# Kernel tuning notes

Hardware: AMD Instinct MI355X
Metric: run time of the kernel (lower is better)

The kernel has to match this reference:

```python
import jax, jax.numpy as jnp
import numpy as np

N = 50000
E = 800000
D_IN = 128
D_HID = 256


def setup_inputs() -> dict:
    key = jax.random.key(0)
    ks = jax.random.split(key, 9)
    x = jax.random.normal(ks[0], (N, D_IN), dtype=jnp.float32)
    edge_index = jax.random.randint(ks[1], (2, E), 0, N, dtype=jnp.int64)
    edge_weight = jax.random.uniform(ks[2], (E,), dtype=jnp.float32)
    # GCNConv params (lin: y = x @ W.T, plus bias added after aggregation)
    W1 = jax.random.normal(ks[3], (D_HID, D_IN), dtype=jnp.float32) / np.sqrt(D_IN)
    b1 = jnp.zeros((D_HID,), dtype=jnp.float32)
    W2 = jax.random.normal(ks[4], (D_IN, D_HID), dtype=jnp.float32) / np.sqrt(D_HID)
    b2 = jnp.zeros((D_IN,), dtype=jnp.float32)
    gamma = jnp.ones((D_IN,), dtype=jnp.float32)
    beta = jnp.zeros((D_IN,), dtype=jnp.float32)
    return {"x": x, "edge_index": edge_index, "edge_weight": edge_weight,
            "W1": W1, "b1": b1, "W2": W2, "b2": b2,
            "gamma": gamma, "beta": beta}


def _gcn_norm(edge_index, edge_weight, n_nodes):
    # add self loops with weight 1.0 (PyG gcn_norm default)
    loop = jnp.arange(n_nodes, dtype=edge_index.dtype)
    src = jnp.concatenate([edge_index[0], loop])
    dst = jnp.concatenate([edge_index[1], loop])
    w = jnp.concatenate([edge_weight, jnp.ones((n_nodes,), edge_weight.dtype)])
    # symmetric normalization: deg over target index
    deg = jax.ops.segment_sum(w, dst, num_segments=n_nodes)
    dinv = jnp.where(deg > 0, jax.lax.rsqrt(deg), 0.0)
    norm = dinv[src] * w * dinv[dst]
    return src, dst, norm


def _gcn_conv(x, src, dst, norm, W, b, n_nodes):
    h = x @ W.T                                    # [N, out]
    msg = h[src] * norm[:, None]                   # gather + scale [E+N, out]
    out = jax.ops.segment_sum(msg, dst, num_segments=n_nodes)
    return out + b


def reference(x, edge_index, edge_weight, W1, b1, W2, b2, gamma, beta):
    n_nodes = x.shape[0]
    src, dst, norm = _gcn_norm(edge_index, edge_weight, n_nodes)
    h = _gcn_conv(x, src, dst, norm, W1, b1, n_nodes)
    h = jax.nn.relu(h)
    h = _gcn_conv(h, src, dst, norm, W2, b2, n_nodes)
    # LayerNorm over last dim
    mu = jnp.mean(h, axis=-1, keepdims=True)
    var = jnp.mean(jnp.square(h - mu), axis=-1, keepdims=True)
    h = (h - mu) * jax.lax.rsqrt(var + 1e-5) * gamma + beta
    return h
```

## Files before the change

kernel.cpp:

```cpp
#include <hip/hip_runtime.h>

typedef unsigned short ushort_t;
typedef __attribute__((ext_vector_type(8))) short short8;
typedef __attribute__((ext_vector_type(4))) float float4v;

#define MAXDEG 48

__device__ inline float b2f(ushort_t u) {
    unsigned x = ((unsigned)u) << 16;
    return __builtin_bit_cast(float, x);
}
__device__ inline ushort_t f2b(float f) {
    unsigned x = __builtin_bit_cast(unsigned, f);
    unsigned r = (x + 0x7fffu + ((x >> 16) & 1u)) >> 16;
    return (ushort_t)r;
}

__device__ inline void load_edge(const int* __restrict__ ei, int e, int E,
                                 int& s, int& d) {
    int ec = min(e, E - 1);
    int2 c64 = ((const int2*)ei)[ec];
    unsigned long long m = __ballot(c64.y != 0);
    if (m != 0ull) {
        s = ei[ec];
        d = ei[(size_t)E + ec];
    } else {
        s = c64.x;
        d = ((const int2*)ei)[(size_t)E + ec].x;
    }
}


__global__ __launch_bounds__(256) void k_mega(const int* __restrict__ ei,
                                              const float* __restrict__ w,
                                              const float* __restrict__ x,
                                              const float* __restrict__ W1,
                                              const float* __restrict__ W2,
                                              unsigned* packed,
                                              unsigned* __restrict__ edata,
                                              ushort_t* __restrict__ xb,
                                              ushort_t* __restrict__ W1b,
                                              ushort_t* __restrict__ W2b,
                                              int E, int Nn, int gE, int gX) {
    int b = blockIdx.x;
    bool isEdge;
    int widx;
    if (3 * gE <= (int)gridDim.x) {
        if (b < 3 * gE) {
            if (b % 3 == 0) { isEdge = true;  widx = b / 3; }
            else            { isEdge = false; widx = b - b / 3 - 1; }
        } else {
            isEdge = false; widx = b - gE;
        }
    } else {
        isEdge = b < gE;
        widx = isEdge ? b : b - gE;
    }

    if (isEdge) {
        int e = widx * 256 + threadIdx.x;
        int s, d;
        load_edge(ei, e, E, s, d);
        if (e < E) {
            if ((unsigned)s < (unsigned)Nn && (unsigned)d < (unsigned)Nn) {
                float wv = w[e];
                unsigned fx = (unsigned)(wv * 65536.0f + 0.5f);
                unsigned old = atomicAdd(packed + d, (1u << 22) | fx);
                int r = (int)(old >> 22);
                if (r < MAXDEG) {
                    unsigned wq = (unsigned)(wv * 32768.0f + 0.5f);
                    wq = min(wq, 32767u);
                    edata[(size_t)d * MAXDEG + r] = ((unsigned)s << 15) | wq;
                }
            }
        }
    } else if (widx < gX) {
        int i = widx * 256 + threadIdx.x;
        if (i < Nn * 32) {
            float4v v = ((const float4v*)x)[i];
            ushort4 o;
            o.x = f2b(v[0]); o.y = f2b(v[1]); o.z = f2b(v[2]); o.w = f2b(v[3]);
            ((ushort4*)xb)[i] = o;
        }
    } else {
        int i = (widx - gX) * 256 + threadIdx.x;
        if (i < 32768) W1b[i] = f2b(W1[i]);
        else if (i < 65536) W2b[i - 32768] = f2b(W2[i - 32768]);
    }
}


__global__ __launch_bounds__(256) void k_dinv(const unsigned* __restrict__ packed,
                                              float* __restrict__ dinv, int Nn) {
    int i = blockIdx.x * 256 + threadIdx.x;
    if (i < Nn) {
        float wsum = (float)(packed[i] & 0x3FFFFFu) * (1.0f / 65536.0f);
        dinv[i] = rsqrtf(1.0f + wsum);
    }
}


__device__ inline void agg_edges(const ushort_t* __restrict__ src,
                                 const unsigned* __restrict__ ed, int n,
                                 const float* __restrict__ dinv,
                                 int hl, float* a) {
    for (int i = 0; i < n; i += 8) {
        unsigned e2[8];
#pragma unroll
        for (int j = 0; j < 8; ++j) e2[j] = ed[min(i + j, n - 1)];
        ushort4 q[8];
        float nw[8];
#pragma unroll
        for (int j = 0; j < 8; ++j) {
            int sN = (int)(e2[j] >> 15);
            q[j] = ((const ushort4*)(src + (size_t)sN * 128))[hl];
            float d = dinv[sN];
            nw[j] = (i + j < n)
                        ? d * (float)(e2[j] & 0x7FFFu) * (1.0f / 32768.0f)
                        : 0.f;
        }
#pragma unroll
        for (int j = 0; j < 8; ++j) {
            a[0] += b2f(q[j].x) * nw[j]; a[1] += b2f(q[j].y) * nw[j];
            a[2] += b2f(q[j].z) * nw[j]; a[3] += b2f(q[j].w) * nw[j];
        }
    }
}


__global__ __launch_bounds__(256) void k_agg1(const ushort_t* __restrict__ xb,
                                              const unsigned* __restrict__ packed,
                                              const unsigned* __restrict__ edata,
                                              const float* __restrict__ dinv,
                                              ushort_t* __restrict__ ax, int Nn) {
    int v = (blockIdx.x * blockDim.x + threadIdx.x) >> 5;
    int hl = threadIdx.x & 31;
    if (v >= Nn) return;
    float dv = dinv[v];
    ushort4 pq = ((const ushort4*)(xb + (size_t)v * 128))[hl];
    float a[4] = {b2f(pq.x) * dv, b2f(pq.y) * dv, b2f(pq.z) * dv, b2f(pq.w) * dv};
    int n = min((int)(packed[v] >> 22), MAXDEG);
    agg_edges(xb, edata + (size_t)v * MAXDEG, n, dinv, hl, a);
    ushort4 o;
    o.x = f2b(a[0] * dv); o.y = f2b(a[1] * dv);
    o.z = f2b(a[2] * dv); o.w = f2b(a[3] * dv);
    ((ushort4*)(ax + (size_t)v * 128))[hl] = o;
}


__global__ __launch_bounds__(256, 2) void k_gemm_fused(const ushort_t* __restrict__ ax,
                                                       const ushort_t* __restrict__ W1b,
                                                       const float* __restrict__ b1v,
                                                       const ushort_t* __restrict__ W2b,
                                                       ushort_t* __restrict__ h2, int Nn) {
    __shared__ ushort_t tile[64][264];
    int tid = threadIdx.x, wid = tid >> 6, lane = tid & 63;
    int m = lane & 15, q = lane >> 4;
    int blk = blockIdx.x * 64;

    short8 wf[4][4];
#pragma unroll
    for (int nt = 0; nt < 4; ++nt) {
        const ushort_t* wb = W1b + (size_t)(wid * 64 + nt * 16 + m) * 128 + q * 8;
#pragma unroll
        for (int kt = 0; kt < 4; ++kt) wf[nt][kt] = *(const short8*)(wb + kt * 32);
    }
    short8 af[4][4];
#pragma unroll
    for (int mi = 0; mi < 4; ++mi) {
        int arow = blk + mi * 16 + m;
        bool rv = arow < Nn;
        const ushort_t* ab = ax + (size_t)arow * 128 + q * 8;
#pragma unroll
        for (int kt = 0; kt < 4; ++kt)
            af[mi][kt] = rv ? *(const short8*)(ab + kt * 32) : (short8)0;
    }

    float4v acc1[4][4];
#pragma unroll
    for (int mi = 0; mi < 4; ++mi)
#pragma unroll
        for (int nt = 0; nt < 4; ++nt) acc1[mi][nt] = (float4v){0.f, 0.f, 0.f, 0.f};

#pragma unroll
    for (int kt = 0; kt < 4; ++kt)
#pragma unroll
        for (int mi = 0; mi < 4; ++mi)
#pragma unroll
            for (int nt = 0; nt < 4; ++nt)
                acc1[mi][nt] = __builtin_amdgcn_mfma_f32_16x16x32_bf16(
                    af[mi][kt], wf[nt][kt], acc1[mi][nt], 0, 0, 0);

#pragma unroll
    for (int nt = 0; nt < 4; ++nt) {
        int col = wid * 64 + nt * 16 + m;
        float bb = b1v[col];
#pragma unroll
        for (int mi = 0; mi < 4; ++mi) {
#pragma unroll
            for (int r = 0; r < 4; ++r) {
                float v = acc1[mi][nt][r] + bb;
                v = v > 0.f ? v : 0.f;
                tile[mi * 16 + q * 4 + r][col] = f2b(v);
            }
        }
    }
    __syncthreads();

    short8 w2f[2][8];
#pragma unroll
    for (int n2 = 0; n2 < 2; ++n2) {
        const ushort_t* wb = W2b + (size_t)(wid * 32 + n2 * 16 + m) * 256 + q * 8;
#pragma unroll
        for (int kt = 0; kt < 8; ++kt) w2f[n2][kt] = *(const short8*)(wb + kt * 32);
    }

    float4v acc2[4][2];
#pragma unroll
    for (int mi = 0; mi < 4; ++mi)
#pragma unroll
        for (int n2 = 0; n2 < 2; ++n2) acc2[mi][n2] = (float4v){0.f, 0.f, 0.f, 0.f};

#pragma unroll
    for (int kt = 0; kt < 8; ++kt) {
#pragma unroll
        for (int mi = 0; mi < 4; ++mi) {
            short8 a2 = *(const short8*)&tile[mi * 16 + m][kt * 32 + q * 8];
#pragma unroll
            for (int n2 = 0; n2 < 2; ++n2)
                acc2[mi][n2] = __builtin_amdgcn_mfma_f32_16x16x32_bf16(
                    a2, w2f[n2][kt], acc2[mi][n2], 0, 0, 0);
        }
    }

#pragma unroll
    for (int mi = 0; mi < 4; ++mi) {
#pragma unroll
        for (int n2 = 0; n2 < 2; ++n2) {
            int col = wid * 32 + n2 * 16 + m;
#pragma unroll
            for (int r = 0; r < 4; ++r) {
                int row = blk + mi * 16 + q * 4 + r;
                if (row < Nn) h2[(size_t)row * 128 + col] = f2b(acc2[mi][n2][r]);
            }
        }
    }
}


__global__ __launch_bounds__(256) void k_agg2_ln(const ushort_t* __restrict__ h2,
                                                 const unsigned* __restrict__ packed,
                                                 const unsigned* __restrict__ edata,
                                                 const float* __restrict__ dinv,
                                                 const float* __restrict__ b2v,
                                                 const float* __restrict__ gv,
                                                 const float* __restrict__ bev,
                                                 float* __restrict__ out, int Nn) {
    int v = (blockIdx.x * blockDim.x + threadIdx.x) >> 5;
    int hl = threadIdx.x & 31;
    if (v >= Nn) return;
    float dv = dinv[v];
    ushort4 pq = ((const ushort4*)(h2 + (size_t)v * 128))[hl];
    float a[4] = {b2f(pq.x) * dv, b2f(pq.y) * dv, b2f(pq.z) * dv, b2f(pq.w) * dv};
    int n = min((int)(packed[v] >> 22), MAXDEG);
    agg_edges(h2, edata + (size_t)v * MAXDEG, n, dinv, hl, a);

    int d0 = hl * 4;
#pragma unroll
    for (int j = 0; j < 4; ++j) {
        a[j] *= dv;
        a[j] += b2v[d0 + j];
    }

    float ssum = a[0] + a[1] + a[2] + a[3];
    float ssq = a[0] * a[0] + a[1] * a[1] + a[2] * a[2] + a[3] * a[3];
#pragma unroll
    for (int off = 1; off < 32; off <<= 1) {
        ssum += __shfl_xor(ssum, off);
        ssq += __shfl_xor(ssq, off);
    }
    float mu = ssum * (1.0f / 128.0f);
    float var = ssq * (1.0f / 128.0f) - mu * mu;
    float r = rsqrtf(var + 1e-5f);
    float4v o;
#pragma unroll
    for (int j = 0; j < 4; ++j)
        o[j] = (a[j] - mu) * r * gv[d0 + j] + bev[d0 + j];
    ((float4v*)(out + (size_t)v * 128))[hl] = o;
}


extern "C" void kernel_launch(void* const* d_in, const int* in_sizes, int n_in,
                              void* d_out, int out_size, void* d_ws, size_t ws_size,
                              hipStream_t stream) {
    const float* x   = (const float*)d_in[0];
    const int*   ei  = (const int*)d_in[1];
    const float* ew  = (const float*)d_in[2];
    const float* W1  = (const float*)d_in[3];
    const float* b1v = (const float*)d_in[4];
    const float* W2  = (const float*)d_in[5];
    const float* b2v = (const float*)d_in[6];
    const float* gv  = (const float*)d_in[7];
    const float* bev = (const float*)d_in[8];
    float* out = (float*)d_out;

    const int Nn = in_sizes[0] / 128;
    const int E  = in_sizes[2];

    char* base = (char*)d_ws;
    size_t off = 0;
    auto alloc = [&](size_t bytes) {
        char* p = base + off;
        off = (off + bytes + 255) & ~(size_t)255;
        return p;
    };
    unsigned* packed = (unsigned*)alloc((size_t)Nn * 4);
    float*    dinv   = (float*)alloc((size_t)Nn * 4);
    unsigned* edata  = (unsigned*)alloc((size_t)Nn * MAXDEG * 4);
    ushort_t* xb     = (ushort_t*)alloc((size_t)Nn * 128 * 2);
    ushort_t* h2     = (ushort_t*)alloc((size_t)Nn * 128 * 2);
    ushort_t* W1b    = (ushort_t*)alloc(32768 * 2);
    ushort_t* W2b    = (ushort_t*)alloc(32768 * 2);
    ushort_t* ax     = (ushort_t*)d_out;
    (void)ws_size; (void)n_in; (void)out_size;

    int gE = (E + 255) / 256;
    int gX = (Nn * 32 + 255) / 256;
    int gW = (Nn + 7) / 8;
    int gG = (Nn + 63) / 64;
    int gD = (Nn + 255) / 256;

    hipMemsetAsync(packed, 0, (size_t)Nn * 4, stream);
    k_mega<<<gE + gX + 256, 256, 0, stream>>>(ei, ew, x, W1, W2, packed, edata,
                                              xb, W1b, W2b, E, Nn, gE, gX);
    k_dinv<<<gD, 256, 0, stream>>>(packed, dinv, Nn);
    k_agg1<<<gW, 256, 0, stream>>>(xb, packed, edata, dinv, ax, Nn);
    k_gemm_fused<<<gG, 256, 0, stream>>>(ax, W1b, b1v, W2b, h2, Nn);
    k_agg2_ln<<<gW, 256, 0, stream>>>(h2, packed, edata, dinv, b2v, gv, bev, out, Nn);
}
```

Before: 241.7 us.

## Pre-scale source features by dinv to drop per-edge dinv gathers

Folds the source-side degree normalization into the node features before aggregation. A new kernel writes x*dinv as bf16, and the fused GEMM scales its h2 output rows by dinv. This removes the random per-edge dinv[src] load from both aggregation kernels, which now recompute dinv from the packed degree word instead of reading the dinv array. The aggregation loop also unrolls the first 16 edges to expose more gathers in flight. The cost is moving the x conversion out of the mega kernel into a separate pass and a possible register-pressure increase from the 16-wide unroll.

```diff
diff --git a/kernel.cpp b/kernel.cpp
--- a/kernel.cpp
+++ b/kernel.cpp
@@ -90,21 +90,47 @@
 }
 
 
-__global__ __launch_bounds__(256) void k_dinv(const unsigned* __restrict__ packed,
-                                              float* __restrict__ dinv, int Nn) {
-    int i = blockIdx.x * 256 + threadIdx.x;
-    if (i < Nn) {
-        float wsum = (float)(packed[i] & 0x3FFFFFu) * (1.0f / 65536.0f);
-        dinv[i] = rsqrtf(1.0f + wsum);
-    }
+__global__ __launch_bounds__(256) void k_xscale(const float* __restrict__ x,
+                                                const unsigned* __restrict__ packed,
+                                                float* __restrict__ dinv,
+                                                ushort_t* __restrict__ xb, int Nn) {
+    int v = (blockIdx.x * blockDim.x + threadIdx.x) >> 5;
+    int hl = threadIdx.x & 31;
+    if (v >= Nn) return;
+    unsigned pk = packed[v];
+    float dv = rsqrtf(1.0f + (float)(pk & 0x3FFFFFu) * (1.0f / 65536.0f));
+    if (hl == 0) dinv[v] = dv;
+    float4v xr = ((const float4v*)(x + (size_t)v * 128))[hl];
+    ushort4 o;
+    o.x = f2b(xr[0] * dv); o.y = f2b(xr[1] * dv);
+    o.z = f2b(xr[2] * dv); o.w = f2b(xr[3] * dv);
+    ((ushort4*)(xb + (size_t)v * 128))[hl] = o;
 }
 
 
 __device__ inline void agg_edges(const ushort_t* __restrict__ src,
                                  const unsigned* __restrict__ ed, int n,
-                                 const float* __restrict__ dinv,
                                  int hl, float* a) {
-    for (int i = 0; i < n; i += 8) {
+    if (n <= 0) return;
+    {
+        unsigned e2[16];
+#pragma unroll
+        for (int j = 0; j < 16; ++j) e2[j] = ed[min(j, n - 1)];
+        ushort4 q[16];
+        float nw[16];
+#pragma unroll
+        for (int j = 0; j < 16; ++j) {
+            int sN = (int)(e2[j] >> 15);
+            q[j] = ((const ushort4*)(src + (size_t)sN * 128))[hl];
+            nw[j] = (j < n) ? (float)(e2[j] & 0x7FFFu) * (1.0f / 32768.0f) : 0.f;
+        }
+#pragma unroll
+        for (int j = 0; j < 16; ++j) {
+            a[0] += b2f(q[j].x) * nw[j]; a[1] += b2f(q[j].y) * nw[j];
+            a[2] += b2f(q[j].z) * nw[j]; a[3] += b2f(q[j].w) * nw[j];
+        }
+    }
+    for (int i = 16; i < n; i += 8) {
         unsigned e2[8];
 #pragma unroll
         for (int j = 0; j < 8; ++j) e2[j] = ed[min(i + j, n - 1)];
@@ -114,10 +140,7 @@
         for (int j = 0; j < 8; ++j) {
             int sN = (int)(e2[j] >> 15);
             q[j] = ((const ushort4*)(src + (size_t)sN * 128))[hl];
-            float d = dinv[sN];
-            nw[j] = (i + j < n)
-                        ? d * (float)(e2[j] & 0x7FFFu) * (1.0f / 32768.0f)
-                        : 0.f;
+            nw[j] = (i + j < n) ? (float)(e2[j] & 0x7FFFu) * (1.0f / 32768.0f) : 0.f;
         }
 #pragma unroll
         for (int j = 0; j < 8; ++j) {
@@ -131,16 +154,16 @@
 __global__ __launch_bounds__(256) void k_agg1(const ushort_t* __restrict__ xb,
                                               const unsigned* __restrict__ packed,
                                               const unsigned* __restrict__ edata,
-                                              const float* __restrict__ dinv,
                                               ushort_t* __restrict__ ax, int Nn) {
     int v = (blockIdx.x * blockDim.x + threadIdx.x) >> 5;
     int hl = threadIdx.x & 31;
     if (v >= Nn) return;
-    float dv = dinv[v];
+    unsigned pk = packed[v];
+    float dv = rsqrtf(1.0f + (float)(pk & 0x3FFFFFu) * (1.0f / 65536.0f));
     ushort4 pq = ((const ushort4*)(xb + (size_t)v * 128))[hl];
-    float a[4] = {b2f(pq.x) * dv, b2f(pq.y) * dv, b2f(pq.z) * dv, b2f(pq.w) * dv};
-    int n = min((int)(packed[v] >> 22), MAXDEG);
-    agg_edges(xb, edata + (size_t)v * MAXDEG, n, dinv, hl, a);
+    float a[4] = {b2f(pq.x), b2f(pq.y), b2f(pq.z), b2f(pq.w)};
+    int n = min((int)(pk >> 22), MAXDEG);
+    agg_edges(xb, edata + (size_t)v * MAXDEG, n, hl, a);
     ushort4 o;
     o.x = f2b(a[0] * dv); o.y = f2b(a[1] * dv);
     o.z = f2b(a[2] * dv); o.w = f2b(a[3] * dv);
@@ -152,6 +175,7 @@
                                                        const ushort_t* __restrict__ W1b,
                                                        const float* __restrict__ b1v,
                                                        const ushort_t* __restrict__ W2b,
+                                                       const float* __restrict__ dinv,
                                                        ushort_t* __restrict__ h2, int Nn) {
     __shared__ ushort_t tile[64][264];
     int tid = threadIdx.x, wid = tid >> 6, lane = tid & 63;
@@ -233,6 +257,15 @@
         }
     }
 
+    float drow[4][4];
+#pragma unroll
+    for (int mi = 0; mi < 4; ++mi)
+#pragma unroll
+        for (int r = 0; r < 4; ++r) {
+            int row = blk + mi * 16 + q * 4 + r;
+            drow[mi][r] = (row < Nn) ? dinv[row] : 0.f;
+        }
+
 #pragma unroll
     for (int mi = 0; mi < 4; ++mi) {
 #pragma unroll
@@ -241,7 +274,8 @@
 #pragma unroll
             for (int r = 0; r < 4; ++r) {
                 int row = blk + mi * 16 + q * 4 + r;
-                if (row < Nn) h2[(size_t)row * 128 + col] = f2b(acc2[mi][n2][r]);
+                if (row < Nn)
+                    h2[(size_t)row * 128 + col] = f2b(acc2[mi][n2][r] * drow[mi][r]);
             }
         }
     }
@@ -251,7 +285,6 @@
 __global__ __launch_bounds__(256) void k_agg2_ln(const ushort_t* __restrict__ h2,
                                                  const unsigned* __restrict__ packed,
                                                  const unsigned* __restrict__ edata,
-                                                 const float* __restrict__ dinv,
                                                  const float* __restrict__ b2v,
                                                  const float* __restrict__ gv,
                                                  const float* __restrict__ bev,
@@ -259,17 +292,17 @@
     int v = (blockIdx.x * blockDim.x + threadIdx.x) >> 5;
     int hl = threadIdx.x & 31;
     if (v >= Nn) return;
-    float dv = dinv[v];
+    unsigned pk = packed[v];
+    float dv = rsqrtf(1.0f + (float)(pk & 0x3FFFFFu) * (1.0f / 65536.0f));
     ushort4 pq = ((const ushort4*)(h2 + (size_t)v * 128))[hl];
-    float a[4] = {b2f(pq.x) * dv, b2f(pq.y) * dv, b2f(pq.z) * dv, b2f(pq.w) * dv};
-    int n = min((int)(packed[v] >> 22), MAXDEG);
-    agg_edges(h2, edata + (size_t)v * MAXDEG, n, dinv, hl, a);
+    float a[4] = {b2f(pq.x), b2f(pq.y), b2f(pq.z), b2f(pq.w)};
+    int n = min((int)(pk >> 22), MAXDEG);
+    agg_edges(h2, edata + (size_t)v * MAXDEG, n, hl, a);
 
     int d0 = hl * 4;
 #pragma unroll
     for (int j = 0; j < 4; ++j) {
-        a[j] *= dv;
-        a[j] += b2v[d0 + j];
+        a[j] = a[j] * dv + b2v[d0 + j];
     }
 
     float ssum = a[0] + a[1] + a[2] + a[3];
@@ -325,16 +358,14 @@
     (void)ws_size; (void)n_in; (void)out_size;
 
     int gE = (E + 255) / 256;
-    int gX = (Nn * 32 + 255) / 256;
     int gW = (Nn + 7) / 8;
     int gG = (Nn + 63) / 64;
-    int gD = (Nn + 255) / 256;
 
     hipMemsetAsync(packed, 0, (size_t)Nn * 4, stream);
-    k_mega<<<gE + gX + 256, 256, 0, stream>>>(ei, ew, x, W1, W2, packed, edata,
-                                              xb, W1b, W2b, E, Nn, gE, gX);
-    k_dinv<<<gD, 256, 0, stream>>>(packed, dinv, Nn);
-    k_agg1<<<gW, 256, 0, stream>>>(xb, packed, edata, dinv, ax, Nn);
-    k_gemm_fused<<<gG, 256, 0, stream>>>(ax, W1b, b1v, W2b, h2, Nn);
-    k_agg2_ln<<<gW, 256, 0, stream>>>(h2, packed, edata, dinv, b2v, gv, bev, out, Nn);
-}
+    k_mega<<<gE + 256, 256, 0, stream>>>(ei, ew, x, W1, W2, packed, edata,
+                                         xb, W1b, W2b, E, Nn, gE, 0);
+    k_xscale<<<gW, 256, 0, stream>>>(x, packed, dinv, xb, Nn);
+    k_agg1<<<gW, 256, 0, stream>>>(xb, packed, edata, ax, Nn);
+    k_gemm_fused<<<gG, 256, 0, stream>>>(ax, W1b, b1v, W2b, dinv, h2, Nn);
+    k_agg2_ln<<<gW, 256, 0, stream>>>(h2, packed, edata, b2v, gv, bev, out, Nn);
+}
```

Measured after the change: 229.1 us. 5.2% less time.
